# Kernel tuning notes

Measured on AMD Instinct MI355X. Metric: run time of the kernel, lower is better.

Reference implementation:

```python
import jax, jax.numpy as jnp
import numpy as np
from jax.scipy.linalg import expm

U_SHAPE = (4, 32, 16, 16, 16, 3, 3)   # [mu, t, x, y, z, 3, 3]
W_SHAPE = (8, 32, 16, 16, 16, 3, 3)   # [feature, t, x, y, z, 3, 3]


def setup_inputs() -> dict:
    key = jax.random.key(0)
    k = jax.random.split(key, 5)
    return {
        "U_re": jax.random.normal(k[0], U_SHAPE, jnp.float32),
        "U_im": jax.random.normal(k[1], U_SHAPE, jnp.float32),
        "W_re": jax.random.normal(k[2], W_SHAPE, jnp.float32),
        "W_im": jax.random.normal(k[3], W_SHAPE, jnp.float32),
        "ah_weights": jax.random.normal(k[4], (4, W_SHAPE[0]), jnp.float32),
    }


def reference(U_re, U_im, W_re, W_im, ah_weights):
    U = (U_re + 1j * U_im).astype(jnp.complex64)
    W = (W_re + 1j * W_im).astype(jnp.complex64)

    # anti-hermitian part: W - W^dagger
    W_adj = jnp.conj(jnp.swapaxes(W, -1, -2))
    A = W - W_adj
    # traceless projection
    tr = jnp.trace(A, axis1=-2, axis2=-1)  # [i,t,x,y,z]
    A = A - (tr / 3.0)[..., None, None] * jnp.eye(3, dtype=A.dtype)

    # exponent: (1j*w) contracted with (-1j*A) == w contracted with A
    E = jnp.einsum('ui,itxyzab->utxyzab', ah_weights.astype(A.dtype), A)

    # batched 3x3 matrix exponential over the whole lattice
    E_flat = E.reshape(-1, 3, 3)
    expE = jax.vmap(expm)(E_flat).reshape(E.shape)

    # apply to gauge links: exp(...) @ U
    return jnp.einsum('utxyzij,utxyzjk->utxyzik', expE, U)
```

## Files before the change

### kernel.cpp

```cpp
#include <hip/hip_runtime.h>
#include <math.h>

#define NSITES 131072
#define PL     (NSITES * 9)

struct cplx { float re, im; };

__device__ __forceinline__ cplx cadd(cplx a, cplx b) { return {a.re + b.re, a.im + b.im}; }
__device__ __forceinline__ cplx cmul(cplx a, cplx b) {
    return { fmaf(a.re, b.re, -(a.im * b.im)), fmaf(a.re, b.im, a.im * b.re) };
}

struct __attribute__((aligned(4))) f3 { float x, y, z; };
__device__ __forceinline__ f3 ld3(const float* __restrict__ p) { return *(const f3*)p; }

struct Acc9 { float r01, r02, r12, i01, i02, i12, d0, d4, d8; };
struct Edof { float er01, er02, er12, ei01, ei02, ei12, ed0, ed1, ed2; };
struct G3   { cplx g0, g1, g2; };
struct C3   { cplx c0, c1, c2; };

__device__ __forceinline__ Edof make_edof(Acc9 a) {
    Edof E;
    E.er01 = a.r01; E.er02 = a.r02; E.er12 = a.r12;
    E.ei01 = a.i01; E.ei02 = a.i02; E.ei12 = a.i12;
    float t3 = (a.d0 + a.d4 + a.d8) * (2.f / 3.f);
    E.ed0 = fmaf(2.f, a.d0, -t3);
    E.ed1 = fmaf(2.f, a.d4, -t3);
    E.ed2 = fmaf(2.f, a.d8, -t3);
    return E;
}

__device__ __forceinline__ G3 expm_coeffs(Edof E)
{
    float r2 = fmaf(E.er01, E.er01, fmaf(E.er02, E.er02, fmaf(E.er12, E.er12,
               fmaf(E.ei01, E.ei01, fmaf(E.ei02, E.ei02, E.ei12 * E.ei12)))));
    r2 = fmaf(2.f, r2, fmaf(E.ed0, E.ed0, fmaf(E.ed1, E.ed1, E.ed2 * E.ed2)));

    const float n01 = fmaf(E.ei01, E.ei01, E.er01 * E.er01);
    const float n02 = fmaf(E.ei02, E.ei02, E.er02 * E.er02);
    const float n12 = fmaf(E.ei12, E.ei12, E.er12 * E.er12);
    const float zre = fmaf(E.ei01, E.ei12, -(E.er01 * E.er12));
    const float zim = -fmaf(E.ei01, E.er12, E.er01 * E.ei12);
    const float detH = E.ed0 * E.ed1 * E.ed2
                     + 2.f * fmaf(zre, E.ei02, -(zim * E.er02))
                     - fmaf(E.ed0, n12, fmaf(E.ed1, n02, E.ed2 * n01));

    int e; (void)frexpf(r2, &e);
    int sc = (e <= -2) ? 0 : min(1 + ((e + 1) >> 1), 40);
    const float inv  = __int_as_float((127 - sc) << 23);
    const float inv2 = inv * inv;
    const float px   = -0.5f * r2 * inv2;
    const float qxi  = -detH * (inv2 * inv);

    cplx T0 = {1.f, 0.f}, T1 = {0.f, 0.f}, T2 = {0.f, 0.f};
    cplx S0 = {1.f, 0.f}, S1 = {0.f, 0.f}, S2 = {0.f, 0.f};
    #pragma unroll
    for (int n = 1; n <= 10; n++) {
        float c  = 1.f / (float)n;
        float qc = qxi * c;
        cplx nT0 = { -qc * T2.im, qc * T2.re };
        cplx nT1 = { c * fmaf(px, T2.re, T0.re), c * fmaf(px, T2.im, T0.im) };
        cplx nT2 = { c * T1.re, c * T1.im };
        T0 = nT0; T1 = nT1; T2 = nT2;
        S0 = cadd(S0, T0); S1 = cadd(S1, T1); S2 = cadd(S2, T2);
    }

    const float q2 = 2.f * qxi;
    for (int k = 0; k < sc; k++) {
        cplx f0 = S0, f1 = S1, f2 = S2;
        cplx f12 = cmul(f1, f2);
        cplx f01 = cmul(f0, f1);
        cplx f02 = cmul(f0, f2);
        float f00re = fmaf(f0.re, f0.re, -(f0.im * f0.im)), f00im = 2.f * f0.re * f0.im;
        float f11re = fmaf(f1.re, f1.re, -(f1.im * f1.im)), f11im = 2.f * f1.re * f1.im;
        float f22re = fmaf(f2.re, f2.re, -(f2.im * f2.im)), f22im = 2.f * f2.re * f2.im;
        S0.re = fmaf(-q2, f12.im, f00re);
        S0.im = fmaf( q2, f12.re, f00im);
        S1.re = fmaf(-qxi, f22im, 2.f * fmaf(px, f12.re, f01.re));
        S1.im = fmaf( qxi, f22re, 2.f * fmaf(px, f12.im, f01.im));
        S2.re = fmaf(px, f22re, fmaf(2.f, f02.re, f11re));
        S2.im = fmaf(px, f22im, fmaf(2.f, f02.im, f11im));
    }
    G3 g;
    g.g0 = S0;
    g.g1 = { S1.re * inv,  S1.im * inv  };
    g.g2 = { S2.re * inv2, S2.im * inv2 };
    return g;
}

__device__ __forceinline__ C3 ecol(Edof E, C3 m)
{
    C3 v;
    v.c0.re = fmaf(-E.ed0, m.c0.im, fmaf(E.er01, m.c1.re, fmaf(-E.ei01, m.c1.im, fmaf(E.er02, m.c2.re, -(E.ei02 * m.c2.im)))));
    v.c0.im = fmaf( E.ed0, m.c0.re, fmaf(E.er01, m.c1.im, fmaf( E.ei01, m.c1.re, fmaf(E.er02, m.c2.im,  (E.ei02 * m.c2.re)))));
    v.c1.re = fmaf(-E.er01, m.c0.re, fmaf(-E.ei01, m.c0.im, fmaf(-E.ed1, m.c1.im, fmaf(E.er12, m.c2.re, -(E.ei12 * m.c2.im)))));
    v.c1.im = fmaf(-E.er01, m.c0.im, fmaf( E.ei01, m.c0.re, fmaf( E.ed1, m.c1.re, fmaf(E.er12, m.c2.im,  (E.ei12 * m.c2.re)))));
    v.c2.re = fmaf(-E.er02, m.c0.re, fmaf(-E.ei02, m.c0.im, fmaf(-E.er12, m.c1.re, fmaf(-E.ei12, m.c1.im, -(E.ed2 * m.c2.im)))));
    v.c2.im = fmaf(-E.er02, m.c0.im, fmaf( E.ei02, m.c0.re, fmaf(-E.er12, m.c1.im, fmaf( E.ei12, m.c1.re,  (E.ed2 * m.c2.re)))));
    return v;
}

__device__ __forceinline__ float ocomb(G3 g, cplx m, cplx v, cplx z) {
    return fmaf(g.g0.re, m.re, fmaf(-g.g0.im, m.im, fmaf(g.g1.re, v.re, fmaf(-g.g1.im, v.im,
           fmaf(g.g2.re, z.re, -(g.g2.im * z.im))))));
}

__device__ __forceinline__ void phase(Acc9 acc,
                                      const float* __restrict__ U_re,
                                      const float* __restrict__ U_im,
                                      float* __restrict__ out, size_t ub)
{
    Edof E = make_edof(acc);
    G3 g = expm_coeffs(E);

    f3 ua = ld3(U_re + ub), ubv = ld3(U_re + ub + 3), uc = ld3(U_re + ub + 6);
    f3 va = ld3(U_im + ub), vb  = ld3(U_im + ub + 3), vc = ld3(U_im + ub + 6);

    float o0,o1,o2,o3,o4,o5,o6,o7,o8;
    {
        C3 m = { cplx{ua.x, va.x}, cplx{ubv.x, vb.x}, cplx{uc.x, vc.x} };
        C3 v = ecol(E, m);
        C3 z = ecol(E, v);
        o0 = ocomb(g, m.c0, v.c0, z.c0);
        o3 = ocomb(g, m.c1, v.c1, z.c1);
        o6 = ocomb(g, m.c2, v.c2, z.c2);
    }
    {
        C3 m = { cplx{ua.y, va.y}, cplx{ubv.y, vb.y}, cplx{uc.y, vc.y} };
        C3 v = ecol(E, m);
        C3 z = ecol(E, v);
        o1 = ocomb(g, m.c0, v.c0, z.c0);
        o4 = ocomb(g, m.c1, v.c1, z.c1);
        o7 = ocomb(g, m.c2, v.c2, z.c2);
    }
    {
        C3 m = { cplx{ua.z, va.z}, cplx{ubv.z, vb.z}, cplx{uc.z, vc.z} };
        C3 v = ecol(E, m);
        C3 z = ecol(E, v);
        o2 = ocomb(g, m.c0, v.c0, z.c0);
        o5 = ocomb(g, m.c1, v.c1, z.c1);
        o8 = ocomb(g, m.c2, v.c2, z.c2);
    }
    float* ob = out + ub;
    *(f3*)(ob)     = { o0, o1, o2 };
    *(f3*)(ob + 3) = { o3, o4, o5 };
    *(f3*)(ob + 6) = { o6, o7, o8 };
}

__global__
__attribute__((amdgpu_flat_work_group_size(256, 256)))
__attribute__((amdgpu_waves_per_eu(2, 2)))
void lge_exp_kernel(
    const float* __restrict__ U_re, const float* __restrict__ U_im,
    const float* __restrict__ W_re, const float* __restrict__ W_im,
    const float* __restrict__ ahw,  float* __restrict__ out)
{
    const int site = blockIdx.x * 256 + threadIdx.x;
    const size_t sb = (size_t)site * 9;

    Acc9 A0 = {0,0,0,0,0,0,0,0,0};
    Acc9 A1 = {0,0,0,0,0,0,0,0,0};
    Acc9 A2 = {0,0,0,0,0,0,0,0,0};
    Acc9 A3 = {0,0,0,0,0,0,0,0,0};

    #pragma unroll
    for (int f = 0; f < 8; f++) {
        const float* pr = W_re + (size_t)f * PL + sb;
        const float* pi = W_im + (size_t)f * PL + sb;
        f3 q  = ld3(pr + 1);
        f3 s  = ld3(pr + 5);
        f3 ia = ld3(pi), ib = ld3(pi + 3), ic = ld3(pi + 6);

        const float p0 = q.x - q.z;
        const float p1 = q.y - s.y;
        const float p2 = s.x - s.z;
        const float p3 = ia.y + ib.x;
        const float p4 = ia.z + ic.x;
        const float p5 = ib.z + ic.y;
        const float p6 = ia.x, p7 = ib.y, p8 = ic.z;

        const float w0 = ahw[0 * 8 + f], w1 = ahw[1 * 8 + f];
        const float w2 = ahw[2 * 8 + f], w3 = ahw[3 * 8 + f];

        A0.r01=fmaf(w0,p0,A0.r01); A0.r02=fmaf(w0,p1,A0.r02); A0.r12=fmaf(w0,p2,A0.r12);
        A0.i01=fmaf(w0,p3,A0.i01); A0.i02=fmaf(w0,p4,A0.i02); A0.i12=fmaf(w0,p5,A0.i12);
        A0.d0 =fmaf(w0,p6,A0.d0);  A0.d4 =fmaf(w0,p7,A0.d4);  A0.d8 =fmaf(w0,p8,A0.d8);

        A1.r01=fmaf(w1,p0,A1.r01); A1.r02=fmaf(w1,p1,A1.r02); A1.r12=fmaf(w1,p2,A1.r12);
        A1.i01=fmaf(w1,p3,A1.i01); A1.i02=fmaf(w1,p4,A1.i02); A1.i12=fmaf(w1,p5,A1.i12);
        A1.d0 =fmaf(w1,p6,A1.d0);  A1.d4 =fmaf(w1,p7,A1.d4);  A1.d8 =fmaf(w1,p8,A1.d8);

        A2.r01=fmaf(w2,p0,A2.r01); A2.r02=fmaf(w2,p1,A2.r02); A2.r12=fmaf(w2,p2,A2.r12);
        A2.i01=fmaf(w2,p3,A2.i01); A2.i02=fmaf(w2,p4,A2.i02); A2.i12=fmaf(w2,p5,A2.i12);
        A2.d0 =fmaf(w2,p6,A2.d0);  A2.d4 =fmaf(w2,p7,A2.d4);  A2.d8 =fmaf(w2,p8,A2.d8);

        A3.r01=fmaf(w3,p0,A3.r01); A3.r02=fmaf(w3,p1,A3.r02); A3.r12=fmaf(w3,p2,A3.r12);
        A3.i01=fmaf(w3,p3,A3.i01); A3.i02=fmaf(w3,p4,A3.i02); A3.i12=fmaf(w3,p5,A3.i12);
        A3.d0 =fmaf(w3,p6,A3.d0);  A3.d4 =fmaf(w3,p7,A3.d4);  A3.d8 =fmaf(w3,p8,A3.d8);
    }

    phase(A0, U_re, U_im, out, ((size_t)0 * NSITES + site) * 9);
    __builtin_amdgcn_sched_barrier(0);
    phase(A1, U_re, U_im, out, ((size_t)1 * NSITES + site) * 9);
    __builtin_amdgcn_sched_barrier(0);
    phase(A2, U_re, U_im, out, ((size_t)2 * NSITES + site) * 9);
    __builtin_amdgcn_sched_barrier(0);
    phase(A3, U_re, U_im, out, ((size_t)3 * NSITES + site) * 9);
}

extern "C" void kernel_launch(void* const* d_in, const int* in_sizes, int n_in,
                              void* d_out, int out_size, void* d_ws, size_t ws_size,
                              hipStream_t stream) {
    const float* U_re = (const float*)d_in[0];
    const float* U_im = (const float*)d_in[1];
    const float* W_re = (const float*)d_in[2];
    const float* W_im = (const float*)d_in[3];
    const float* ahw  = (const float*)d_in[4];
    float* out = (float*)d_out;
    lge_exp_kernel<<<dim3(NSITES / 256), dim3(256), 0, stream>>>(
        U_re, U_im, W_re, W_im, ahw, out);
}
```

Baseline: 143.9 us.

## Split each site across two threads, each handling two mu directions

Two threads now share each lattice site, and each one computes the exponentials for two of the four mu directions instead of all four. This halves register pressure per thread, so occupancy is raised to 4 waves per EU and the grid doubles. The U loads are also moved ahead of the expm coefficient computation so they can overlap with arithmetic. The cost is that both threads of a pair load and combine the same W data, which doubles W reads (mostly served by cache since neighbouring lanes share them) and the projection arithmetic.

```diff
diff --git a/kernel.cpp b/kernel.cpp
--- a/kernel.cpp
+++ b/kernel.cpp
@@ -110,11 +110,11 @@
                                       const float* __restrict__ U_im,
                                       float* __restrict__ out, size_t ub)
 {
+    f3 ua = ld3(U_re + ub), ubv = ld3(U_re + ub + 3), uc = ld3(U_re + ub + 6);
+    f3 va = ld3(U_im + ub), vb  = ld3(U_im + ub + 3), vc = ld3(U_im + ub + 6);
+
     Edof E = make_edof(acc);
     G3 g = expm_coeffs(E);
-
-    f3 ua = ld3(U_re + ub), ubv = ld3(U_re + ub + 3), uc = ld3(U_re + ub + 6);
-    f3 va = ld3(U_im + ub), vb  = ld3(U_im + ub + 3), vc = ld3(U_im + ub + 6);
 
     float o0,o1,o2,o3,o4,o5,o6,o7,o8;
     {
@@ -149,19 +149,19 @@
 
 __global__
 __attribute__((amdgpu_flat_work_group_size(256, 256)))
-__attribute__((amdgpu_waves_per_eu(2, 2)))
+__attribute__((amdgpu_waves_per_eu(4, 4)))
 void lge_exp_kernel(
     const float* __restrict__ U_re, const float* __restrict__ U_im,
     const float* __restrict__ W_re, const float* __restrict__ W_im,
     const float* __restrict__ ahw,  float* __restrict__ out)
 {
-    const int site = blockIdx.x * 256 + threadIdx.x;
+    const int gid  = blockIdx.x * 256 + threadIdx.x;
+    const int site = gid >> 1;
+    const int half = gid & 1;
     const size_t sb = (size_t)site * 9;
 
     Acc9 A0 = {0,0,0,0,0,0,0,0,0};
     Acc9 A1 = {0,0,0,0,0,0,0,0,0};
-    Acc9 A2 = {0,0,0,0,0,0,0,0,0};
-    Acc9 A3 = {0,0,0,0,0,0,0,0,0};
 
     #pragma unroll
     for (int f = 0; f < 8; f++) {
@@ -179,33 +179,21 @@
         const float p5 = ib.z + ic.y;
         const float p6 = ia.x, p7 = ib.y, p8 = ic.z;
 
-        const float w0 = ahw[0 * 8 + f], w1 = ahw[1 * 8 + f];
-        const float w2 = ahw[2 * 8 + f], w3 = ahw[3 * 8 + f];
-
-        A0.r01=fmaf(w0,p0,A0.r01); A0.r02=fmaf(w0,p1,A0.r02); A0.r12=fmaf(w0,p2,A0.r12);
-        A0.i01=fmaf(w0,p3,A0.i01); A0.i02=fmaf(w0,p4,A0.i02); A0.i12=fmaf(w0,p5,A0.i12);
-        A0.d0 =fmaf(w0,p6,A0.d0);  A0.d4 =fmaf(w0,p7,A0.d4);  A0.d8 =fmaf(w0,p8,A0.d8);
-
-        A1.r01=fmaf(w1,p0,A1.r01); A1.r02=fmaf(w1,p1,A1.r02); A1.r12=fmaf(w1,p2,A1.r12);
-        A1.i01=fmaf(w1,p3,A1.i01); A1.i02=fmaf(w1,p4,A1.i02); A1.i12=fmaf(w1,p5,A1.i12);
-        A1.d0 =fmaf(w1,p6,A1.d0);  A1.d4 =fmaf(w1,p7,A1.d4);  A1.d8 =fmaf(w1,p8,A1.d8);
-
-        A2.r01=fmaf(w2,p0,A2.r01); A2.r02=fmaf(w2,p1,A2.r02); A2.r12=fmaf(w2,p2,A2.r12);
-        A2.i01=fmaf(w2,p3,A2.i01); A2.i02=fmaf(w2,p4,A2.i02); A2.i12=fmaf(w2,p5,A2.i12);
-        A2.d0 =fmaf(w2,p6,A2.d0);  A2.d4 =fmaf(w2,p7,A2.d4);  A2.d8 =fmaf(w2,p8,A2.d8);
-
-        A3.r01=fmaf(w3,p0,A3.r01); A3.r02=fmaf(w3,p1,A3.r02); A3.r12=fmaf(w3,p2,A3.r12);
-        A3.i01=fmaf(w3,p3,A3.i01); A3.i02=fmaf(w3,p4,A3.i02); A3.i12=fmaf(w3,p5,A3.i12);
-        A3.d0 =fmaf(w3,p6,A3.d0);  A3.d4 =fmaf(w3,p7,A3.d4);  A3.d8 =fmaf(w3,p8,A3.d8);
-    }
-
-    phase(A0, U_re, U_im, out, ((size_t)0 * NSITES + site) * 9);
+        const float wA = half ? ahw[1 * 8 + f] : ahw[0 * 8 + f];
+        const float wB = half ? ahw[3 * 8 + f] : ahw[2 * 8 + f];
+
+        A0.r01=fmaf(wA,p0,A0.r01); A0.r02=fmaf(wA,p1,A0.r02); A0.r12=fmaf(wA,p2,A0.r12);
+        A0.i01=fmaf(wA,p3,A0.i01); A0.i02=fmaf(wA,p4,A0.i02); A0.i12=fmaf(wA,p5,A0.i12);
+        A0.d0 =fmaf(wA,p6,A0.d0);  A0.d4 =fmaf(wA,p7,A0.d4);  A0.d8 =fmaf(wA,p8,A0.d8);
+
+        A1.r01=fmaf(wB,p0,A1.r01); A1.r02=fmaf(wB,p1,A1.r02); A1.r12=fmaf(wB,p2,A1.r12);
+        A1.i01=fmaf(wB,p3,A1.i01); A1.i02=fmaf(wB,p4,A1.i02); A1.i12=fmaf(wB,p5,A1.i12);
+        A1.d0 =fmaf(wB,p6,A1.d0);  A1.d4 =fmaf(wB,p7,A1.d4);  A1.d8 =fmaf(wB,p8,A1.d8);
+    }
+
+    phase(A0, U_re, U_im, out, ((size_t)half * NSITES + site) * 9);
     __builtin_amdgcn_sched_barrier(0);
-    phase(A1, U_re, U_im, out, ((size_t)1 * NSITES + site) * 9);
-    __builtin_amdgcn_sched_barrier(0);
-    phase(A2, U_re, U_im, out, ((size_t)2 * NSITES + site) * 9);
-    __builtin_amdgcn_sched_barrier(0);
-    phase(A3, U_re, U_im, out, ((size_t)3 * NSITES + site) * 9);
+    phase(A1, U_re, U_im, out, ((size_t)(half + 2) * NSITES + site) * 9);
 }
 
 extern "C" void kernel_launch(void* const* d_in, const int* in_sizes, int n_in,
@@ -217,6 +205,6 @@
     const float* W_im = (const float*)d_in[3];
     const float* ahw  = (const float*)d_in[4];
     float* out = (float*)d_out;
-    lge_exp_kernel<<<dim3(NSITES / 256), dim3(256), 0, stream>>>(
+    lge_exp_kernel<<<dim3(NSITES * 2 / 256), dim3(256), 0, stream>>>(
         U_re, U_im, W_re, W_im, ahw, out);
 }
```

Measured after the change: 155.0 us. +7.7%, slower.
